# Performance work log

Measured on AMD Instinct MI355X. Metric: run time of the kernel, lower is better.

The kernel has to match this reference:

```python
import jax, jax.numpy as jnp
import numpy as np

NUM_HEADS = 4
OUT_DIM = 64
IN_DIM = 128

def setup_inputs() -> dict:
    key = jax.random.key(0)
    k1, k2, k3, k4 = jax.random.split(key, 4)
    h = jax.random.normal(k1, (4, 256, IN_DIM), dtype=jnp.float32)
    adj = jax.random.randint(k2, (4, 256, 256), 0, 2).astype(jnp.int32)
    W = jax.random.normal(k3, (IN_DIM, NUM_HEADS * OUT_DIM), dtype=jnp.float32) * (1.0 / np.sqrt(IN_DIM))
    a = jax.random.normal(k4, (2 * OUT_DIM, 1), dtype=jnp.float32) * 0.1
    return {"h": h, "adj": adj, "W": W, "a": a}

def reference(h, adj, W, a):
    B, N, _ = h.shape
    H, D = NUM_HEADS, OUT_DIM
    Wh = (h @ W).reshape(B, N, H, D)                      # [B,N,H,D]
    # Exact replication of the torch repeat/view construction (row-major, same as torch.view)
    a1 = jnp.tile(Wh, (1, 1, 1, N)).reshape(B, N * H, N, D)
    a2 = jnp.tile(Wh, (1, N, 1, 1)).reshape(B, N * H, N, D)
    a_input = jnp.concatenate([a1, a2], axis=3)           # [B,N*H,N,2D]
    e = jax.nn.leaky_relu((a_input @ a)[..., 0], negative_slope=0.2)
    e = e.reshape(B, H, N, N)
    mask = adj[:, None, :, :] == 0                        # broadcast over heads
    attention = jax.nn.softmax(jnp.where(mask, -jnp.inf, e), axis=3)  # [B,H,N,N]
    h_prime = jnp.einsum('bhij,bjhd->bihd', attention, Wh)             # [B,N,H,D]
    return h_prime.reshape(B, N, H * D)
```

## Files before the change

### kernel.cpp

```cpp
#include <hip/hip_runtime.h>


typedef __attribute__((ext_vector_type(8))) short bf16x8;
typedef __attribute__((ext_vector_type(4))) float f32x4;

__device__ __forceinline__ short bf1(float x) {
  unsigned u = __builtin_bit_cast(unsigned, x);
  u = (u + 0x7FFFu + ((u >> 16) & 1u)) >> 16;
  return (short)u;
}
__device__ __forceinline__ bf16x8 pack8(float4 a, float4 b) {
  bf16x8 r;
  r[0]=bf1(a.x); r[1]=bf1(a.y); r[2]=bf1(a.z); r[3]=bf1(a.w);
  r[4]=bf1(b.x); r[5]=bf1(b.y); r[6]=bf1(b.z); r[7]=bf1(b.w);
  return r;
}

__global__ __launch_bounds__(256) void gat_prep(
    const float* __restrict__ h, const float* __restrict__ W,
    const float* __restrict__ a, const int* __restrict__ adj,
    short* __restrict__ WhT, float* __restrict__ f1g, float* __restrict__ f2g)
{
  const int tid  = threadIdx.x;
  const int lane = tid & 63;
  const int quad = lane >> 4, col = lane & 15;
  const int wv   = tid >> 6;
  const int blk  = blockIdx.x;
  const int ms = blk & 15, nt = (blk >> 4) & 3, b = blk >> 6;

  __shared__ short WbT[64][136];
  __shared__ short WaT16[16][136];

  const int4 aw = ((const int4*)adj)[blk * 256 + tid];

  float4 wl[8];
#pragma unroll
  for (int q = 0; q < 8; q++) {
    const int idx = q * 256 + tid;
    const int k = idx >> 4, c4 = idx & 15;
    wl[q] = *(const float4*)(W + k * 256 + nt * 64 + c4 * 4);
  }
  const float* hrow = h + (b*256 + ms*16 + col) * 128 + quad*8;
  float4 hv[8];
#pragma unroll
  for (int kk = 0; kk < 4; kk++) {
    hv[2*kk]   = *(const float4*)(hrow + kk*32);
    hv[2*kk+1] = *(const float4*)(hrow + kk*32 + 4);
  }

  {
    const int k = tid >> 1, s = tid & 1;
    const float4* wr = (const float4*)(W + k * 256 + nt * 64);
    const float4* av = (const float4*)(a + s * 64);
    float sacc = 0.f;
#pragma unroll
    for (int d4 = 0; d4 < 16; d4++) {
      float4 x = wr[d4]; float4 y = av[d4];
      sacc += x.x*y.x + x.y*y.y + x.z*y.z + x.w*y.w;
    }
    WaT16[s][k] = bf1(sacc);
    int* zp = (int*)&WaT16[2][0];
    for (int t = tid; t < 952; t += 256) zp[t] = 0;
  }

#pragma unroll
  for (int q = 0; q < 8; q++) {
    const int idx = q * 256 + tid;
    const int k = idx >> 4, c4 = idx & 15;
    WbT[c4*4 + 0][k] = bf1(wl[q].x);
    WbT[c4*4 + 1][k] = bf1(wl[q].y);
    WbT[c4*4 + 2][k] = bf1(wl[q].z);
    WbT[c4*4 + 3][k] = bf1(wl[q].w);
  }
  __syncthreads();

  bf16x8 afr[4];
#pragma unroll
  for (int kk = 0; kk < 4; kk++) afr[kk] = pack8(hv[2*kk], hv[2*kk+1]);

  f32x4 acc = {0.f, 0.f, 0.f, 0.f};
#pragma unroll
  for (int kk = 0; kk < 4; kk++) {
    bf16x8 bw = *(const bf16x8*)&WbT[wv*16 + col][kk*32 + quad*8];
    acc = __builtin_amdgcn_mfma_f32_16x16x32_bf16(afr[kk], bw, acc, 0, 0, 0);
  }
  {
    const int dcol = nt*64 + wv*16 + col;
    const int n0   = ms*16 + quad*4;
    int2 pk;
    pk.x = (int)((unsigned)(unsigned short)bf1(acc[0]) |
                 ((unsigned)(unsigned short)bf1(acc[1]) << 16));
    pk.y = (int)((unsigned)(unsigned short)bf1(acc[2]) |
                 ((unsigned)(unsigned short)bf1(acc[3]) << 16));
    *(int2*)(WhT + b*65536 + dcol*256 + n0) = pk;
  }

  if (wv == 0) {
    f32x4 accF = {0.f, 0.f, 0.f, 0.f};
#pragma unroll
    for (int kk = 0; kk < 4; kk++) {
      bf16x8 bw = *(const bf16x8*)&WaT16[col][kk*32 + quad*8];
      accF = __builtin_amdgcn_mfma_f32_16x16x32_bf16(afr[kk], bw, accF, 0, 0, 0);
    }
    if (col < 2) {
      float* dst = (col == 0) ? f1g : f2g;
#pragma unroll
      for (int r = 0; r < 4; r++)
        dst[b*1024 + (ms*16 + quad*4 + r)*4 + nt] = accF[r];
    }
  }

  asm volatile("" :: "v"(aw.x), "v"(aw.y), "v"(aw.z), "v"(aw.w));
}

__global__ __launch_bounds__(256) void gat_attn(
    const short* __restrict__ WhT, const float* __restrict__ f1g,
    const float* __restrict__ f2g, const int* __restrict__ adj,
    float* __restrict__ out)
{
  const int tid  = threadIdx.x;
  const int lane = tid & 63;
  const int quad = lane >> 4, col = lane & 15;
  const int wv   = tid >> 6;
  const int blk  = blockIdx.x;
  const int it = blk & 15, hp = (blk >> 4) & 3, b = blk >> 6;
  const int i0 = it * 16;

  __shared__ short attb[16][264];

  bf16x8 bv[8];
  const short* bp = WhT + b*65536 + (hp*64 + wv*16 + col)*256 + quad*8;
#pragma unroll
  for (int kk = 0; kk < 8; kk++) bv[kk] = *(const bf16x8*)(bp + kk*32);

  float4 f2v[4]; int4 av[4]; float f1s[4];
#pragma unroll
  for (int rq = 0; rq < 4; rq++) {
    const int i = i0 + wv*4 + rq;
    f2v[rq] = *(const float4*)(f2g + b*1024 + rq*256 + lane*4);
    av[rq]  = *(const int4*)(adj + (b*256 + i)*256 + lane*4);
    f1s[rq] = f1g[b*1024 + hp*256 + i];
  }

#pragma unroll
  for (int rq = 0; rq < 4; rq++) {
    const int rr = wv*4 + rq;
    const float s1v = f1s[rq];
    float e0 = s1v + f2v[rq].x, e1 = s1v + f2v[rq].y;
    float e2 = s1v + f2v[rq].z, e3 = s1v + f2v[rq].w;
    e0 = e0 > 0.f ? e0 : 0.2f*e0;  e1 = e1 > 0.f ? e1 : 0.2f*e1;
    e2 = e2 > 0.f ? e2 : 0.2f*e2;  e3 = e3 > 0.f ? e3 : 0.2f*e3;
    e0 = av[rq].x ? e0 : -1e30f;  e1 = av[rq].y ? e1 : -1e30f;
    e2 = av[rq].z ? e2 : -1e30f;  e3 = av[rq].w ? e3 : -1e30f;
    float x0 = __expf(e0), x1 = __expf(e1);
    float x2 = __expf(e2), x3 = __expf(e3);
    int2 pk2;
    pk2.x = (int)((unsigned)(unsigned short)bf1(x0) |
                  ((unsigned)(unsigned short)bf1(x1) << 16));
    pk2.y = (int)((unsigned)(unsigned short)bf1(x2) |
                  ((unsigned)(unsigned short)bf1(x3) << 16));
    *(int2*)&attb[rr][lane*4] = pk2;
  }
  __syncthreads();

  bf16x8 af[8];
#pragma unroll
  for (int kk = 0; kk < 8; kk++)
    af[kk] = *(const bf16x8*)&attb[col][kk*32 + quad*8];

  bf16x8 ones;
#pragma unroll
  for (int j = 0; j < 8; j++) ones[j] = (short)0x3F80;

  f32x4 acc0 = {0.f,0.f,0.f,0.f}, acc1 = {0.f,0.f,0.f,0.f};
  f32x4 sum0 = {0.f,0.f,0.f,0.f}, sum1 = {0.f,0.f,0.f,0.f};
#pragma unroll
  for (int kk = 0; kk < 4; kk++) {
    acc0 = __builtin_amdgcn_mfma_f32_16x16x32_bf16(af[kk],   bv[kk],   acc0, 0, 0, 0);
    acc1 = __builtin_amdgcn_mfma_f32_16x16x32_bf16(af[kk+4], bv[kk+4], acc1, 0, 0, 0);
    sum0 = __builtin_amdgcn_mfma_f32_16x16x32_bf16(af[kk],   ones,     sum0, 0, 0, 0);
    sum1 = __builtin_amdgcn_mfma_f32_16x16x32_bf16(af[kk+4], ones,     sum1, 0, 0, 0);
  }
#pragma unroll
  for (int r = 0; r < 4; r++) {
    const int m = quad*4 + r;
    out[(b*256 + i0 + m)*256 + hp*64 + wv*16 + col] =
        (acc0[r] + acc1[r]) / (sum0[r] + sum1[r]);
  }
}

extern "C" void kernel_launch(void* const* d_in, const int* in_sizes, int n_in,
                              void* d_out, int out_size, void* d_ws, size_t ws_size,
                              hipStream_t stream) {
  const float* h   = (const float*)d_in[0];
  const int*   adj = (const int*)d_in[1];
  const float* W   = (const float*)d_in[2];
  const float* a   = (const float*)d_in[3];
  float* out = (float*)d_out;

  short* WhT = (short*)d_ws;
  float* f1g = (float*)((char*)d_ws + 4*256*256*2);
  float* f2g = f1g + 4*1024;

  gat_prep<<<256, 256, 0, stream>>>(h, W, a, adj, WhT, f1g, f2g);
  gat_attn<<<256, 256, 0, stream>>>(WhT, f1g, f2g, adj, out);
}
```

Before: 65.23 us.

## Fuse prep and attention kernels with a grid-wide atomic barrier

Merges the projection kernel and the attention kernel into one launch of 256 blocks, separated by a global atomic-counter barrier with a generation-based base. The adjacency rows are loaded at kernel start and held in registers across the barrier, so their latency overlaps the projection phase. This removes the second kernel launch and the inter-kernel gap. In exchange it relies on all 256 blocks being co-resident, adds spin-wait cost at the barrier, and raises register pressure from the held adjacency values.

```diff
diff --git a/kernel.cpp b/kernel.cpp
--- a/kernel.cpp
+++ b/kernel.cpp
@@ -3,6 +3,8 @@
 
 typedef __attribute__((ext_vector_type(8))) short bf16x8;
 typedef __attribute__((ext_vector_type(4))) float f32x4;
+
+__device__ unsigned g_ctr = 0;
 
 __device__ __forceinline__ short bf1(float x) {
   unsigned u = __builtin_bit_cast(unsigned, x);
@@ -16,10 +18,11 @@
   return r;
 }
 
-__global__ __launch_bounds__(256) void gat_prep(
+__global__ __launch_bounds__(256) void gat_fused(
     const float* __restrict__ h, const float* __restrict__ W,
     const float* __restrict__ a, const int* __restrict__ adj,
-    short* __restrict__ WhT, float* __restrict__ f1g, float* __restrict__ f2g)
+    short* __restrict__ WhT, float* __restrict__ f1g, float* __restrict__ f2g,
+    float* __restrict__ out)
 {
   const int tid  = threadIdx.x;
   const int lane = tid & 63;
@@ -27,165 +30,171 @@
   const int wv   = tid >> 6;
   const int blk  = blockIdx.x;
   const int ms = blk & 15, nt = (blk >> 4) & 3, b = blk >> 6;
+  const int i0 = ms * 16;
 
   __shared__ short WbT[64][136];
   __shared__ short WaT16[16][136];
-
-  const int4 aw = ((const int4*)adj)[blk * 256 + tid];
-
-  float4 wl[8];
-#pragma unroll
-  for (int q = 0; q < 8; q++) {
-    const int idx = q * 256 + tid;
-    const int k = idx >> 4, c4 = idx & 15;
-    wl[q] = *(const float4*)(W + k * 256 + nt * 64 + c4 * 4);
+  __shared__ short attb[16][264];
+
+  int4 adjv[4];
+#pragma unroll
+  for (int rq = 0; rq < 4; rq++)
+    adjv[rq] = *(const int4*)(adj + (b*256 + i0 + wv*4 + rq)*256 + lane*4);
+
+  {
+    float4 wl[8];
+#pragma unroll
+    for (int q = 0; q < 8; q++) {
+      const int idx = q * 256 + tid;
+      const int k = idx >> 4, c4 = idx & 15;
+      wl[q] = *(const float4*)(W + k * 256 + nt * 64 + c4 * 4);
+    }
+    const float* hrow = h + (b*256 + ms*16 + col) * 128 + quad*8;
+    float4 hv[8];
+#pragma unroll
+    for (int kk = 0; kk < 4; kk++) {
+      hv[2*kk]   = *(const float4*)(hrow + kk*32);
+      hv[2*kk+1] = *(const float4*)(hrow + kk*32 + 4);
+    }
+
+    {
+      const int k = tid >> 1, s = tid & 1;
+      const float4* wr = (const float4*)(W + k * 256 + nt * 64);
+      const float4* av = (const float4*)(a + s * 64);
+      float sacc = 0.f;
+#pragma unroll
+      for (int d4 = 0; d4 < 16; d4++) {
+        float4 x = wr[d4]; float4 y = av[d4];
+        sacc += x.x*y.x + x.y*y.y + x.z*y.z + x.w*y.w;
+      }
+      WaT16[s][k] = bf1(sacc);
+      int* zp = (int*)&WaT16[2][0];
+      for (int t = tid; t < 952; t += 256) zp[t] = 0;
+    }
+
+#pragma unroll
+    for (int q = 0; q < 8; q++) {
+      const int idx = q * 256 + tid;
+      const int k = idx >> 4, c4 = idx & 15;
+      WbT[c4*4 + 0][k] = bf1(wl[q].x);
+      WbT[c4*4 + 1][k] = bf1(wl[q].y);
+      WbT[c4*4 + 2][k] = bf1(wl[q].z);
+      WbT[c4*4 + 3][k] = bf1(wl[q].w);
+    }
+    __syncthreads();
+
+    bf16x8 afr[4];
+#pragma unroll
+    for (int kk = 0; kk < 4; kk++) afr[kk] = pack8(hv[2*kk], hv[2*kk+1]);
+
+    f32x4 acc = {0.f, 0.f, 0.f, 0.f};
+#pragma unroll
+    for (int kk = 0; kk < 4; kk++) {
+      bf16x8 bw = *(const bf16x8*)&WbT[wv*16 + col][kk*32 + quad*8];
+      acc = __builtin_amdgcn_mfma_f32_16x16x32_bf16(afr[kk], bw, acc, 0, 0, 0);
+    }
+    {
+      const int dcol = nt*64 + wv*16 + col;
+      const int n0   = ms*16 + quad*4;
+      int2 pk;
+      pk.x = (int)((unsigned)(unsigned short)bf1(acc[0]) |
+                   ((unsigned)(unsigned short)bf1(acc[1]) << 16));
+      pk.y = (int)((unsigned)(unsigned short)bf1(acc[2]) |
+                   ((unsigned)(unsigned short)bf1(acc[3]) << 16));
+      *(int2*)(WhT + b*65536 + dcol*256 + n0) = pk;
+    }
+
+    if (wv == 0) {
+      f32x4 accF = {0.f, 0.f, 0.f, 0.f};
+#pragma unroll
+      for (int kk = 0; kk < 4; kk++) {
+        bf16x8 bw = *(const bf16x8*)&WaT16[col][kk*32 + quad*8];
+        accF = __builtin_amdgcn_mfma_f32_16x16x32_bf16(afr[kk], bw, accF, 0, 0, 0);
+      }
+      if (col < 2) {
+        float* dst = (col == 0) ? f1g : f2g;
+#pragma unroll
+        for (int r = 0; r < 4; r++)
+          dst[b*1024 + (ms*16 + quad*4 + r)*4 + nt] = accF[r];
+      }
+    }
   }
-  const float* hrow = h + (b*256 + ms*16 + col) * 128 + quad*8;
-  float4 hv[8];
-#pragma unroll
-  for (int kk = 0; kk < 4; kk++) {
-    hv[2*kk]   = *(const float4*)(hrow + kk*32);
-    hv[2*kk+1] = *(const float4*)(hrow + kk*32 + 4);
-  }
-
-  {
-    const int k = tid >> 1, s = tid & 1;
-    const float4* wr = (const float4*)(W + k * 256 + nt * 64);
-    const float4* av = (const float4*)(a + s * 64);
-    float sacc = 0.f;
-#pragma unroll
-    for (int d4 = 0; d4 < 16; d4++) {
-      float4 x = wr[d4]; float4 y = av[d4];
-      sacc += x.x*y.x + x.y*y.y + x.z*y.z + x.w*y.w;
-    }
-    WaT16[s][k] = bf1(sacc);
-    int* zp = (int*)&WaT16[2][0];
-    for (int t = tid; t < 952; t += 256) zp[t] = 0;
-  }
-
-#pragma unroll
-  for (int q = 0; q < 8; q++) {
-    const int idx = q * 256 + tid;
-    const int k = idx >> 4, c4 = idx & 15;
-    WbT[c4*4 + 0][k] = bf1(wl[q].x);
-    WbT[c4*4 + 1][k] = bf1(wl[q].y);
-    WbT[c4*4 + 2][k] = bf1(wl[q].z);
-    WbT[c4*4 + 3][k] = bf1(wl[q].w);
+
+  __threadfence();
+  __syncthreads();
+  if (tid == 0) {
+    const unsigned t    = __hip_atomic_fetch_add(&g_ctr, 1u, __ATOMIC_ACQ_REL,
+                                                 __HIP_MEMORY_SCOPE_AGENT);
+    const unsigned base = t & ~255u;
+    while (__hip_atomic_load(&g_ctr, __ATOMIC_ACQUIRE,
+                             __HIP_MEMORY_SCOPE_AGENT) - base < 256u) {
+      __builtin_amdgcn_s_sleep(1);
+    }
   }
   __syncthreads();
-
-  bf16x8 afr[4];
-#pragma unroll
-  for (int kk = 0; kk < 4; kk++) afr[kk] = pack8(hv[2*kk], hv[2*kk+1]);
-
-  f32x4 acc = {0.f, 0.f, 0.f, 0.f};
-#pragma unroll
-  for (int kk = 0; kk < 4; kk++) {
-    bf16x8 bw = *(const bf16x8*)&WbT[wv*16 + col][kk*32 + quad*8];
-    acc = __builtin_amdgcn_mfma_f32_16x16x32_bf16(afr[kk], bw, acc, 0, 0, 0);
-  }
+  (void)__hip_atomic_load(&g_ctr, __ATOMIC_ACQUIRE, __HIP_MEMORY_SCOPE_AGENT);
+
   {
-    const int dcol = nt*64 + wv*16 + col;
-    const int n0   = ms*16 + quad*4;
-    int2 pk;
-    pk.x = (int)((unsigned)(unsigned short)bf1(acc[0]) |
-                 ((unsigned)(unsigned short)bf1(acc[1]) << 16));
-    pk.y = (int)((unsigned)(unsigned short)bf1(acc[2]) |
-                 ((unsigned)(unsigned short)bf1(acc[3]) << 16));
-    *(int2*)(WhT + b*65536 + dcol*256 + n0) = pk;
-  }
-
-  if (wv == 0) {
-    f32x4 accF = {0.f, 0.f, 0.f, 0.f};
+    const int hp = nt;
+
+    bf16x8 bv[8];
+    const short* bp = WhT + b*65536 + (hp*64 + wv*16 + col)*256 + quad*8;
+#pragma unroll
+    for (int kk = 0; kk < 8; kk++) bv[kk] = *(const bf16x8*)(bp + kk*32);
+
+    float4 f2v[4]; float f1s[4];
+#pragma unroll
+    for (int rq = 0; rq < 4; rq++) {
+      const int i = i0 + wv*4 + rq;
+      f2v[rq] = *(const float4*)(f2g + b*1024 + rq*256 + lane*4);
+      f1s[rq] = f1g[b*1024 + hp*256 + i];
+    }
+
+#pragma unroll
+    for (int rq = 0; rq < 4; rq++) {
+      const int rr = wv*4 + rq;
+      const float s1v = f1s[rq];
+      float e0 = s1v + f2v[rq].x, e1 = s1v + f2v[rq].y;
+      float e2 = s1v + f2v[rq].z, e3 = s1v + f2v[rq].w;
+      e0 = e0 > 0.f ? e0 : 0.2f*e0;  e1 = e1 > 0.f ? e1 : 0.2f*e1;
+      e2 = e2 > 0.f ? e2 : 0.2f*e2;  e3 = e3 > 0.f ? e3 : 0.2f*e3;
+      e0 = adjv[rq].x ? e0 : -1e30f;  e1 = adjv[rq].y ? e1 : -1e30f;
+      e2 = adjv[rq].z ? e2 : -1e30f;  e3 = adjv[rq].w ? e3 : -1e30f;
+      float x0 = __expf(e0), x1 = __expf(e1);
+      float x2 = __expf(e2), x3 = __expf(e3);
+      int2 pk2;
+      pk2.x = (int)((unsigned)(unsigned short)bf1(x0) |
+                    ((unsigned)(unsigned short)bf1(x1) << 16));
+      pk2.y = (int)((unsigned)(unsigned short)bf1(x2) |
+                    ((unsigned)(unsigned short)bf1(x3) << 16));
+      *(int2*)&attb[rr][lane*4] = pk2;
+    }
+    __syncthreads();
+
+    bf16x8 af[8];
+#pragma unroll
+    for (int kk = 0; kk < 8; kk++)
+      af[kk] = *(const bf16x8*)&attb[col][kk*32 + quad*8];
+
+    bf16x8 ones;
+#pragma unroll
+    for (int j = 0; j < 8; j++) ones[j] = (short)0x3F80;
+
+    f32x4 acc0 = {0.f,0.f,0.f,0.f}, acc1 = {0.f,0.f,0.f,0.f};
+    f32x4 sum0 = {0.f,0.f,0.f,0.f}, sum1 = {0.f,0.f,0.f,0.f};
 #pragma unroll
     for (int kk = 0; kk < 4; kk++) {
-      bf16x8 bw = *(const bf16x8*)&WaT16[col][kk*32 + quad*8];
-      accF = __builtin_amdgcn_mfma_f32_16x16x32_bf16(afr[kk], bw, accF, 0, 0, 0);
-    }
-    if (col < 2) {
-      float* dst = (col == 0) ? f1g : f2g;
-#pragma unroll
-      for (int r = 0; r < 4; r++)
-        dst[b*1024 + (ms*16 + quad*4 + r)*4 + nt] = accF[r];
-    }
-  }
-
-  asm volatile("" :: "v"(aw.x), "v"(aw.y), "v"(aw.z), "v"(aw.w));
-}
-
-__global__ __launch_bounds__(256) void gat_attn(
-    const short* __restrict__ WhT, const float* __restrict__ f1g,
-    const float* __restrict__ f2g, const int* __restrict__ adj,
-    float* __restrict__ out)
-{
-  const int tid  = threadIdx.x;
-  const int lane = tid & 63;
-  const int quad = lane >> 4, col = lane & 15;
-  const int wv   = tid >> 6;
-  const int blk  = blockIdx.x;
-  const int it = blk & 15, hp = (blk >> 4) & 3, b = blk >> 6;
-  const int i0 = it * 16;
-
-  __shared__ short attb[16][264];
-
-  bf16x8 bv[8];
-  const short* bp = WhT + b*65536 + (hp*64 + wv*16 + col)*256 + quad*8;
-#pragma unroll
-  for (int kk = 0; kk < 8; kk++) bv[kk] = *(const bf16x8*)(bp + kk*32);
-
-  float4 f2v[4]; int4 av[4]; float f1s[4];
-#pragma unroll
-  for (int rq = 0; rq < 4; rq++) {
-    const int i = i0 + wv*4 + rq;
-    f2v[rq] = *(const float4*)(f2g + b*1024 + rq*256 + lane*4);
-    av[rq]  = *(const int4*)(adj + (b*256 + i)*256 + lane*4);
-    f1s[rq] = f1g[b*1024 + hp*256 + i];
-  }
-
-#pragma unroll
-  for (int rq = 0; rq < 4; rq++) {
-    const int rr = wv*4 + rq;
-    const float s1v = f1s[rq];
-    float e0 = s1v + f2v[rq].x, e1 = s1v + f2v[rq].y;
-    float e2 = s1v + f2v[rq].z, e3 = s1v + f2v[rq].w;
-    e0 = e0 > 0.f ? e0 : 0.2f*e0;  e1 = e1 > 0.f ? e1 : 0.2f*e1;
-    e2 = e2 > 0.f ? e2 : 0.2f*e2;  e3 = e3 > 0.f ? e3 : 0.2f*e3;
-    e0 = av[rq].x ? e0 : -1e30f;  e1 = av[rq].y ? e1 : -1e30f;
-    e2 = av[rq].z ? e2 : -1e30f;  e3 = av[rq].w ? e3 : -1e30f;
-    float x0 = __expf(e0), x1 = __expf(e1);
-    float x2 = __expf(e2), x3 = __expf(e3);
-    int2 pk2;
-    pk2.x = (int)((unsigned)(unsigned short)bf1(x0) |
-                  ((unsigned)(unsigned short)bf1(x1) << 16));
-    pk2.y = (int)((unsigned)(unsigned short)bf1(x2) |
-                  ((unsigned)(unsigned short)bf1(x3) << 16));
-    *(int2*)&attb[rr][lane*4] = pk2;
-  }
-  __syncthreads();
-
-  bf16x8 af[8];
-#pragma unroll
-  for (int kk = 0; kk < 8; kk++)
-    af[kk] = *(const bf16x8*)&attb[col][kk*32 + quad*8];
-
-  bf16x8 ones;
-#pragma unroll
-  for (int j = 0; j < 8; j++) ones[j] = (short)0x3F80;
-
-  f32x4 acc0 = {0.f,0.f,0.f,0.f}, acc1 = {0.f,0.f,0.f,0.f};
-  f32x4 sum0 = {0.f,0.f,0.f,0.f}, sum1 = {0.f,0.f,0.f,0.f};
-#pragma unroll
-  for (int kk = 0; kk < 4; kk++) {
-    acc0 = __builtin_amdgcn_mfma_f32_16x16x32_bf16(af[kk],   bv[kk],   acc0, 0, 0, 0);
-    acc1 = __builtin_amdgcn_mfma_f32_16x16x32_bf16(af[kk+4], bv[kk+4], acc1, 0, 0, 0);
-    sum0 = __builtin_amdgcn_mfma_f32_16x16x32_bf16(af[kk],   ones,     sum0, 0, 0, 0);
-    sum1 = __builtin_amdgcn_mfma_f32_16x16x32_bf16(af[kk+4], ones,     sum1, 0, 0, 0);
-  }
-#pragma unroll
-  for (int r = 0; r < 4; r++) {
-    const int m = quad*4 + r;
-    out[(b*256 + i0 + m)*256 + hp*64 + wv*16 + col] =
-        (acc0[r] + acc1[r]) / (sum0[r] + sum1[r]);
+      acc0 = __builtin_amdgcn_mfma_f32_16x16x32_bf16(af[kk],   bv[kk],   acc0, 0, 0, 0);
+      acc1 = __builtin_amdgcn_mfma_f32_16x16x32_bf16(af[kk+4], bv[kk+4], acc1, 0, 0, 0);
+      sum0 = __builtin_amdgcn_mfma_f32_16x16x32_bf16(af[kk],   ones,     sum0, 0, 0, 0);
+      sum1 = __builtin_amdgcn_mfma_f32_16x16x32_bf16(af[kk+4], ones,     sum1, 0, 0, 0);
+    }
+#pragma unroll
+    for (int r = 0; r < 4; r++) {
+      const int m = quad*4 + r;
+      out[(b*256 + i0 + m)*256 + hp*64 + wv*16 + col] =
+          (acc0[r] + acc1[r]) / (sum0[r] + sum1[r]);
+    }
   }
 }
 
@@ -202,6 +211,5 @@
   float* f1g = (float*)((char*)d_ws + 4*256*256*2);
   float* f2g = f1g + 4*1024;
 
-  gat_prep<<<256, 256, 0, stream>>>(h, W, a, adj, WhT, f1g, f2g);
-  gat_attn<<<256, 256, 0, stream>>>(WhT, f1g, f2g, adj, out);
-}
+  gat_fused<<<256, 256, 0, stream>>>(h, W, a, adj, WhT, f1g, f2g, out);
+}
```

New measurement: 110.5 us. 69.4% more time.
